# Kernel optimization log

Hardware: AMD Instinct MI355X
Metric: run time of the kernel (lower is better)

Reference implementation:

```python
import jax, jax.numpy as jnp
import numpy as np

B, N, E, F, H, K, C, G = 64, 2048, 16384, 32, 64, 8, 16, 64


def setup_inputs() -> dict:
    key = jax.random.key(0)
    ks = jax.random.split(key, 10)
    s = lambda fan: 1.0 / np.sqrt(fan)
    return {
        "x": jax.random.normal(ks[0], (B, N, C), jnp.float32),
        "linc": (jax.random.uniform(ks[1], (N, E)) < (8.0 / N)).astype(jnp.float32),
        "rinc": (jax.random.uniform(ks[2], (E, N)) < (8.0 / N)).astype(jnp.float32),
        "ef": jax.random.normal(ks[3], (E, F), jnp.float32),
        "w1": jax.random.uniform(ks[4], (H, F), jnp.float32, -s(F), s(F)),
        "b1": jax.random.uniform(ks[5], (H,), jnp.float32, -s(F), s(F)),
        "w2": jax.random.uniform(ks[6], (K, H), jnp.float32, -s(H), s(H)),
        "b2": jax.random.uniform(ks[7], (K,), jnp.float32, -s(H), s(H)),
        "gcw": jax.random.uniform(ks[8], (G, C * K), jnp.float32, -s(C * K), s(C * K)),
        "gcb": jax.random.uniform(ks[9], (G,), jnp.float32, -s(C * K), s(C * K)),
    }


def reference(x, linc, rinc, ef, w1, b1, w2, b2, gcw, gcb):
    # edge MLP -> per-edge kernel weights [E, K]
    h = jax.nn.relu(ef @ w1.T + b1)
    w = h @ w2.T + b2
    # structurally: y_k = linc @ diag(w[:,k]) @ rinc @ x, without building [K,N,N]
    z = jnp.einsum('en,bnc->bec', rinc, x)                  # gather: node -> edge
    y = jnp.einsum('ne,ek,bec->bnck', linc, w, z)           # scale + scatter: edge -> node
    b = x.shape[0]
    y = y.reshape(b, N, C * K)                              # matches permute(0,2,-1,1).reshape
    out = jax.nn.relu(y @ gcw.T + gcb)                      # [B, N, G]
    return out.reshape(b, -1)
```

## Files before the change

kernel.cpp:

```cpp
#include <hip/hip_runtime.h>
#include <hip/hip_bf16.h>

#define B_ 64
#define N_ 2048
#define E_ 16384
#define F_ 32
#define H_ 64
#define K_ 8
#define C_ 16
#define G_ 64
#define CK 128
#define CAP 120
#define RCAP 32
#define YLD 136
#define BC 1024

typedef __attribute__((ext_vector_type(8))) short bf16x8;
typedef __attribute__((ext_vector_type(8))) unsigned short u16x8;
typedef __attribute__((ext_vector_type(4))) float f32x4;

__device__ inline float bf2f(unsigned short u) {
  union { unsigned int i; float f; } v; v.i = ((unsigned int)u) << 16; return v.f;
}
__device__ inline unsigned short f2bf(float f) {
  union { float f; unsigned int i; } v; v.f = f;
  unsigned int x = v.i;
  return (unsigned short)((x + 0x7fffu + ((x >> 16) & 1u)) >> 16);
}

__global__ __launch_bounds__(256) void prep_k(
    const float* __restrict__ x, const float* __restrict__ gcw,
    const float* __restrict__ ef, const float* __restrict__ w1,
    const float* __restrict__ b1, const float* __restrict__ w2,
    const float* __restrict__ b2, const float* __restrict__ linc,
    unsigned short* __restrict__ x_t, unsigned short* __restrict__ gcw_bf,
    float* __restrict__ w_out, int* __restrict__ lcnt,
    unsigned short* __restrict__ lidx) {
  int t = threadIdx.x;
  int blk = blockIdx.x;

  if (blk < N_) {
    int n = blk;
    int b = t >> 2, c0 = (t & 3) * 4;
    f32x4 xv = __builtin_nontemporal_load(
        (const f32x4*)(x + (size_t)b*(N_*C_) + (size_t)n*C_ + c0));
    ushort4 o;
    o.x = f2bf(xv.x); o.y = f2bf(xv.y); o.z = f2bf(xv.z); o.w = f2bf(xv.w);
    *(ushort4*)&x_t[(size_t)n*BC + 4*t] = o;
    return;
  }
  if (blk == N_) {
    for (int i = t; i < G_*CK; i += 256) gcw_bf[i] = f2bf(gcw[i]);
    return;
  }
  if (blk <= N_ + E_/256) {
    __shared__ float s_w1[H_*F_];
    __shared__ float s_w2[K_*H_];
    __shared__ float s_b1[H_];
    __shared__ float s_b2[K_];
    for (int i = t; i < H_*F_; i += 256) s_w1[i] = w1[i];
    for (int i = t; i < K_*H_; i += 256) s_w2[i] = w2[i];
    if (t < H_) s_b1[t] = b1[t];
    if (t < K_) s_b2[t] = b2[t];
    __syncthreads();
    int e = (blk - N_ - 1)*256 + t;
    float efr[F_];
    const float4* efp = (const float4*)(ef + (size_t)e*F_);
    #pragma unroll
    for (int f4 = 0; f4 < F_/4; f4++) {
      float4 v = efp[f4];
      efr[f4*4+0]=v.x; efr[f4*4+1]=v.y; efr[f4*4+2]=v.z; efr[f4*4+3]=v.w;
    }
    float acc[K_];
    #pragma unroll
    for (int k = 0; k < K_; k++) acc[k] = s_b2[k];
    #pragma unroll 4
    for (int h = 0; h < H_; h++) {
      float hv = s_b1[h];
      #pragma unroll
      for (int f = 0; f < F_; f++) hv = fmaf(efr[f], s_w1[h*F_+f], hv);
      hv = fmaxf(hv, 0.f);
      #pragma unroll
      for (int k = 0; k < K_; k++) acc[k] = fmaf(hv, s_w2[k*H_+h], acc[k]);
    }
    #pragma unroll
    for (int k = 0; k < K_; k++) w_out[(size_t)e*K_ + k] = acc[k];
    return;
  }
  {
    __shared__ unsigned short s_list[CAP];
    __shared__ int s_cnt;
    int n = blk - (N_ + E_/256 + 1);
    if (t == 0) s_cnt = 0;
    __syncthreads();
    const f32x4* row = (const f32x4*)(linc + (size_t)n*E_);
    #pragma unroll
    for (int j = 0; j < E_/4/256; j++) {
      int i = t + 256*j;
      f32x4 v = __builtin_nontemporal_load(row + i);
      if (v.x != 0.f) { int p = atomicAdd(&s_cnt,1); if (p<CAP) s_list[p] = (unsigned short)(i*4+0); }
      if (v.y != 0.f) { int p = atomicAdd(&s_cnt,1); if (p<CAP) s_list[p] = (unsigned short)(i*4+1); }
      if (v.z != 0.f) { int p = atomicAdd(&s_cnt,1); if (p<CAP) s_list[p] = (unsigned short)(i*4+2); }
      if (v.w != 0.f) { int p = atomicAdd(&s_cnt,1); if (p<CAP) s_list[p] = (unsigned short)(i*4+3); }
    }
    __syncthreads();
    int cnt = min(s_cnt, CAP);
    if (t == 0) lcnt[n] = cnt;
    for (int i = t; i < cnt; i += 256) lidx[(size_t)n*CAP + i] = s_list[i];
  }
}

__global__ __launch_bounds__(256) void scan_gather_k(
    const float* __restrict__ rinc, const unsigned short* __restrict__ x_t,
    unsigned short* __restrict__ z) {
  __shared__ unsigned short s_list[8][RCAP];
  __shared__ int s_cnt[8];
  int t = threadIdx.x;
  int e0 = blockIdx.x * 8;
  if (t < 8) s_cnt[t] = 0;
  __syncthreads();
  const f32x4* base = (const f32x4*)(rinc + (size_t)e0*N_);
  #pragma unroll
  for (int j = 0; j < 8*N_/4/256; j++) {
    int i = t + 256*j;
    f32x4 v = __builtin_nontemporal_load(base + i);
    int er = i >> 9;
    int nn = (i & 511) * 4;
    if (v.x != 0.f) { int p = atomicAdd(&s_cnt[er],1); if (p<RCAP) s_list[er][p] = (unsigned short)(nn+0); }
    if (v.y != 0.f) { int p = atomicAdd(&s_cnt[er],1); if (p<RCAP) s_list[er][p] = (unsigned short)(nn+1); }
    if (v.z != 0.f) { int p = atomicAdd(&s_cnt[er],1); if (p<RCAP) s_list[er][p] = (unsigned short)(nn+2); }
    if (v.w != 0.f) { int p = atomicAdd(&s_cnt[er],1); if (p<RCAP) s_list[er][p] = (unsigned short)(nn+3); }
  }
  __syncthreads();
  int wv = t >> 6, lane = t & 63;
  const unsigned short* xb = x_t + 16*lane;
  #pragma unroll
  for (int rep = 0; rep < 2; rep++) {
    int er = wv + 4*rep;
    int e = e0 + er;
    int cnt = min(s_cnt[er], RCAP);
    float acc[16];
    #pragma unroll
    for (int k = 0; k < 16; k++) acc[k] = 0.f;
    #pragma unroll 2
    for (int i = 0; i < cnt; i++) {
      int n = s_list[er][i];
      u16x8 a0 = *(const u16x8*)(xb + (size_t)n*BC);
      u16x8 a1 = *(const u16x8*)(xb + (size_t)n*BC + 8);
      #pragma unroll
      for (int k = 0; k < 8; k++) { acc[k] += bf2f(a0[k]); acc[8+k] += bf2f(a1[k]); }
    }
    u16x8 o0, o1;
    #pragma unroll
    for (int k = 0; k < 8; k++) { o0[k] = f2bf(acc[k]); o1[k] = f2bf(acc[8+k]); }
    unsigned short* zp = z + (size_t)e*BC + 16*lane;
    __builtin_nontemporal_store(o0, (u16x8*)zp);
    __builtin_nontemporal_store(o1, (u16x8*)(zp + 8));
  }
}

__global__ __launch_bounds__(256, 6) void node_out_k(
    const int* __restrict__ lcnt, const unsigned short* __restrict__ lidx,
    const unsigned short* __restrict__ z, const float* __restrict__ w,
    const unsigned short* __restrict__ gcw_bf, const float* __restrict__ gcb,
    float* __restrict__ out) {
  __shared__ unsigned short s_y[B_*YLD];
  __shared__ float s_w[CAP*K_];
  __shared__ float s_gcb[G_];
  __shared__ int   s_idx[CAP];
  int t = threadIdx.x;
  int n = blockIdx.x;
  if (t < G_) s_gcb[t] = gcb[t];

  int cnt = min(lcnt[n], CAP);
  const unsigned short* lrow = lidx + (size_t)n*CAP;
  for (int i = t; i < cnt; i += 256) s_idx[i] = lrow[i];
  __syncthreads();
  for (int i = t; i < cnt*K_; i += 256)
    s_w[i] = w[(size_t)s_idx[i >> 3]*K_ + (i & 7)];
  __syncthreads();

  float acc[4][K_];
  #pragma unroll
  for (int j = 0; j < 4; j++)
    #pragma unroll
    for (int k = 0; k < K_; k++) acc[j][k] = 0.f;
  const unsigned short* zt = z + 4*t;
  int i = 0;
  for (; i + 4 <= cnt; i += 4) {
    int e0 = s_idx[i], e1 = s_idx[i+1], e2 = s_idx[i+2], e3 = s_idx[i+3];
    ushort4 zu0 = *(const ushort4*)(zt + (size_t)e0*BC);
    ushort4 zu1 = *(const ushort4*)(zt + (size_t)e1*BC);
    ushort4 zu2 = *(const ushort4*)(zt + (size_t)e2*BC);
    ushort4 zu3 = *(const ushort4*)(zt + (size_t)e3*BC);
    #pragma unroll
    for (int u = 0; u < 4; u++) {
      ushort4 zu = (u==0) ? zu0 : (u==1) ? zu1 : (u==2) ? zu2 : zu3;
      const float4* wp = (const float4*)&s_w[(i+u)*K_];
      float4 w0 = wp[0], w1v = wp[1];
      float we[K_] = {w0.x, w0.y, w0.z, w0.w, w1v.x, w1v.y, w1v.z, w1v.w};
      float zv[4] = {bf2f(zu.x), bf2f(zu.y), bf2f(zu.z), bf2f(zu.w)};
      #pragma unroll
      for (int j = 0; j < 4; j++)
        #pragma unroll
        for (int k = 0; k < K_; k++) acc[j][k] = fmaf(zv[j], we[k], acc[j][k]);
    }
  }
  for (; i < cnt; i++) {
    int e = s_idx[i];
    const float4* wp = (const float4*)&s_w[i*K_];
    float4 w0 = wp[0], w1v = wp[1];
    float we[K_] = {w0.x, w0.y, w0.z, w0.w, w1v.x, w1v.y, w1v.z, w1v.w};
    ushort4 zu = *(const ushort4*)(zt + (size_t)e*BC);
    float zv[4] = {bf2f(zu.x), bf2f(zu.y), bf2f(zu.z), bf2f(zu.w)};
    #pragma unroll
    for (int j = 0; j < 4; j++)
      #pragma unroll
      for (int k = 0; k < K_; k++) acc[j][k] = fmaf(zv[j], we[k], acc[j][k]);
  }
  {
    int b = t >> 2, ckb = (t & 3) * 32;
    #pragma unroll
    for (int j = 0; j < 4; j++) {
      ushort4 lo, hi;
      lo.x = f2bf(acc[j][0]); lo.y = f2bf(acc[j][1]); lo.z = f2bf(acc[j][2]); lo.w = f2bf(acc[j][3]);
      hi.x = f2bf(acc[j][4]); hi.y = f2bf(acc[j][5]); hi.z = f2bf(acc[j][6]); hi.w = f2bf(acc[j][7]);
      *(ushort4*)&s_y[b*YLD + ckb + 8*j]     = lo;
      *(ushort4*)&s_y[b*YLD + ckb + 8*j + 4] = hi;
    }
  }
  __syncthreads();

  {
    int wv = t >> 6, lane = t & 63;
    int m = lane & 15, q = lane >> 4;
    f32x4 cf0 = {0.f,0.f,0.f,0.f}, cf1 = cf0, cf2 = cf0, cf3 = cf0;
    #pragma unroll
    for (int ks = 0; ks < 4; ks++) {
      bf16x8 a = *(const bf16x8*)&s_y[(16*wv + m)*YLD + 32*ks + 8*q];
      bf16x8 b0 = *(const bf16x8*)&gcw_bf[(size_t)(m     )*CK + 32*ks + 8*q];
      bf16x8 b1 = *(const bf16x8*)&gcw_bf[(size_t)(16 + m)*CK + 32*ks + 8*q];
      bf16x8 b2 = *(const bf16x8*)&gcw_bf[(size_t)(32 + m)*CK + 32*ks + 8*q];
      bf16x8 b3 = *(const bf16x8*)&gcw_bf[(size_t)(48 + m)*CK + 32*ks + 8*q];
      cf0 = __builtin_amdgcn_mfma_f32_16x16x32_bf16(a, b0, cf0, 0, 0, 0);
      cf1 = __builtin_amdgcn_mfma_f32_16x16x32_bf16(a, b1, cf1, 0, 0, 0);
      cf2 = __builtin_amdgcn_mfma_f32_16x16x32_bf16(a, b2, cf2, 0, 0, 0);
      cf3 = __builtin_amdgcn_mfma_f32_16x16x32_bf16(a, b3, cf3, 0, 0, 0);
    }
    float* ob = out + (size_t)n*G_;
    #pragma unroll
    for (int r = 0; r < 4; r++) {
      int b = 16*wv + 4*q + r;
      float* op = ob + (size_t)b*(N_*G_);
      float v0 = fmaxf(cf0[r] + s_gcb[m],      0.f);
      float v1 = fmaxf(cf1[r] + s_gcb[16 + m], 0.f);
      float v2 = fmaxf(cf2[r] + s_gcb[32 + m], 0.f);
      float v3 = fmaxf(cf3[r] + s_gcb[48 + m], 0.f);
      op[m]      = v0;
      op[16 + m] = v1;
      op[32 + m] = v2;
      op[48 + m] = v3;
    }
  }
}

extern "C" void kernel_launch(void* const* d_in, const int* in_sizes, int n_in,
                              void* d_out, int out_size, void* d_ws, size_t ws_size,
                              hipStream_t stream) {
  const float* x    = (const float*)d_in[0];
  const float* linc = (const float*)d_in[1];
  const float* rinc = (const float*)d_in[2];
  const float* ef   = (const float*)d_in[3];
  const float* w1   = (const float*)d_in[4];
  const float* b1   = (const float*)d_in[5];
  const float* w2   = (const float*)d_in[6];
  const float* b2   = (const float*)d_in[7];
  const float* gcw  = (const float*)d_in[8];
  const float* gcb  = (const float*)d_in[9];
  float* out = (float*)d_out;

  char* ws = (char*)d_ws;
  float* w_e             = (float*)ws;            ws += (size_t)E_*K_*sizeof(float);
  unsigned short* z      = (unsigned short*)ws;   ws += (size_t)E_*BC*sizeof(short);
  unsigned short* x_t    = (unsigned short*)ws;   ws += (size_t)N_*BC*sizeof(short);
  unsigned short* gcw_bf = (unsigned short*)ws;   ws += (size_t)G_*CK*sizeof(short);
  int* lcnt              = (int*)ws;              ws += (size_t)N_*sizeof(int);
  unsigned short* lidx   = (unsigned short*)ws;   ws += (size_t)N_*CAP*sizeof(short);

  prep_k<<<N_ + 1 + E_/256 + N_, 256, 0, stream>>>(
      x, gcw, ef, w1, b1, w2, b2, linc, x_t, gcw_bf, w_e, lcnt, lidx);
  scan_gather_k<<<E_/8, 256, 0, stream>>>(rinc, x_t, z);
  node_out_k<<<N_, 256, 0, stream>>>(lcnt, lidx, z, w_e, gcw_bf, gcb, out);
}
```

Before: 360.2 us.

## Rebalance kernels: run linc scan and edge MLP alongside the rinc gather

Moves the linc row scan and the edge MLP out of the prep kernel into the gather kernel's grid, so the prep kernel only transposes x and converts gcw. The two large dense streams, rinc (for the gather) and linc, now run concurrently in one launch instead of being split across a dependency boundary, which should improve bandwidth overlap and shorten the critical path. The z stores also change from nontemporal to regular stores, so z may stay in cache for node_out_k. The cost is a more heterogeneous grid, where the long scan blocks can leave a tail.

```diff
diff --git a/kernel.cpp b/kernel.cpp
--- a/kernel.cpp
+++ b/kernel.cpp
@@ -28,32 +28,103 @@
   return (unsigned short)((x + 0x7fffu + ((x >> 16) & 1u)) >> 16);
 }
 
-__global__ __launch_bounds__(256) void prep_k(
+__global__ __launch_bounds__(256) void xpose_k(
     const float* __restrict__ x, const float* __restrict__ gcw,
-    const float* __restrict__ ef, const float* __restrict__ w1,
-    const float* __restrict__ b1, const float* __restrict__ w2,
-    const float* __restrict__ b2, const float* __restrict__ linc,
-    unsigned short* __restrict__ x_t, unsigned short* __restrict__ gcw_bf,
-    float* __restrict__ w_out, int* __restrict__ lcnt,
-    unsigned short* __restrict__ lidx) {
+    unsigned short* __restrict__ x_t, unsigned short* __restrict__ gcw_bf) {
   int t = threadIdx.x;
   int blk = blockIdx.x;
-
-  if (blk < N_) {
-    int n = blk;
-    int b = t >> 2, c0 = (t & 3) * 4;
-    f32x4 xv = __builtin_nontemporal_load(
-        (const f32x4*)(x + (size_t)b*(N_*C_) + (size_t)n*C_ + c0));
-    ushort4 o;
-    o.x = f2bf(xv.x); o.y = f2bf(xv.y); o.z = f2bf(xv.z); o.w = f2bf(xv.w);
-    *(ushort4*)&x_t[(size_t)n*BC + 4*t] = o;
-    return;
-  }
   if (blk == N_) {
     for (int i = t; i < G_*CK; i += 256) gcw_bf[i] = f2bf(gcw[i]);
     return;
   }
-  if (blk <= N_ + E_/256) {
+  int n = blk;
+  int b = t >> 2, c0 = (t & 3) * 4;
+  f32x4 xv = __builtin_nontemporal_load(
+      (const f32x4*)(x + (size_t)b*(N_*C_) + (size_t)n*C_ + c0));
+  ushort4 o;
+  o.x = f2bf(xv.x); o.y = f2bf(xv.y); o.z = f2bf(xv.z); o.w = f2bf(xv.w);
+  *(ushort4*)&x_t[(size_t)n*BC + 4*t] = o;
+}
+
+__global__ __launch_bounds__(256) void streams_k(
+    const float* __restrict__ rinc, const unsigned short* __restrict__ x_t,
+    unsigned short* __restrict__ z, const float* __restrict__ linc,
+    int* __restrict__ lcnt, unsigned short* __restrict__ lidx,
+    const float* __restrict__ ef, const float* __restrict__ w1,
+    const float* __restrict__ b1, const float* __restrict__ w2,
+    const float* __restrict__ b2, float* __restrict__ w_out) {
+  int t = threadIdx.x;
+  int blk = blockIdx.x;
+
+  if (blk < E_/8) {
+    __shared__ unsigned short s_list[8][RCAP];
+    __shared__ int s_cnt[8];
+    int e0 = blk * 8;
+    if (t < 8) s_cnt[t] = 0;
+    __syncthreads();
+    const f32x4* base = (const f32x4*)(rinc + (size_t)e0*N_);
+    #pragma unroll
+    for (int j = 0; j < 8*N_/4/256; j++) {
+      int i = t + 256*j;
+      f32x4 v = __builtin_nontemporal_load(base + i);
+      int er = i >> 9;
+      int nn = (i & 511) * 4;
+      if (v.x != 0.f) { int p = atomicAdd(&s_cnt[er],1); if (p<RCAP) s_list[er][p] = (unsigned short)(nn+0); }
+      if (v.y != 0.f) { int p = atomicAdd(&s_cnt[er],1); if (p<RCAP) s_list[er][p] = (unsigned short)(nn+1); }
+      if (v.z != 0.f) { int p = atomicAdd(&s_cnt[er],1); if (p<RCAP) s_list[er][p] = (unsigned short)(nn+2); }
+      if (v.w != 0.f) { int p = atomicAdd(&s_cnt[er],1); if (p<RCAP) s_list[er][p] = (unsigned short)(nn+3); }
+    }
+    __syncthreads();
+    int wv = t >> 6, lane = t & 63;
+    const unsigned short* xb = x_t + 16*lane;
+    #pragma unroll
+    for (int rep = 0; rep < 2; rep++) {
+      int er = wv + 4*rep;
+      int e = e0 + er;
+      int cnt = min(s_cnt[er], RCAP);
+      float acc[16];
+      #pragma unroll
+      for (int k = 0; k < 16; k++) acc[k] = 0.f;
+      #pragma unroll 2
+      for (int i = 0; i < cnt; i++) {
+        int n = s_list[er][i];
+        u16x8 a0 = *(const u16x8*)(xb + (size_t)n*BC);
+        u16x8 a1 = *(const u16x8*)(xb + (size_t)n*BC + 8);
+        #pragma unroll
+        for (int k = 0; k < 8; k++) { acc[k] += bf2f(a0[k]); acc[8+k] += bf2f(a1[k]); }
+      }
+      u16x8 o0, o1;
+      #pragma unroll
+      for (int k = 0; k < 8; k++) { o0[k] = f2bf(acc[k]); o1[k] = f2bf(acc[8+k]); }
+      unsigned short* zp = z + (size_t)e*BC + 16*lane;
+      *(u16x8*)zp = o0;
+      *(u16x8*)(zp + 8) = o1;
+    }
+    return;
+  }
+  if (blk < E_/8 + N_) {
+    __shared__ unsigned short s_list[CAP];
+    __shared__ int s_cnt;
+    int n = blk - E_/8;
+    if (t == 0) s_cnt = 0;
+    __syncthreads();
+    const f32x4* row = (const f32x4*)(linc + (size_t)n*E_);
+    #pragma unroll
+    for (int j = 0; j < E_/4/256; j++) {
+      int i = t + 256*j;
+      f32x4 v = __builtin_nontemporal_load(row + i);
+      if (v.x != 0.f) { int p = atomicAdd(&s_cnt,1); if (p<CAP) s_list[p] = (unsigned short)(i*4+0); }
+      if (v.y != 0.f) { int p = atomicAdd(&s_cnt,1); if (p<CAP) s_list[p] = (unsigned short)(i*4+1); }
+      if (v.z != 0.f) { int p = atomicAdd(&s_cnt,1); if (p<CAP) s_list[p] = (unsigned short)(i*4+2); }
+      if (v.w != 0.f) { int p = atomicAdd(&s_cnt,1); if (p<CAP) s_list[p] = (unsigned short)(i*4+3); }
+    }
+    __syncthreads();
+    int cnt = min(s_cnt, CAP);
+    if (t == 0) lcnt[n] = cnt;
+    for (int i = t; i < cnt; i += 256) lidx[(size_t)n*CAP + i] = s_list[i];
+    return;
+  }
+  {
     __shared__ float s_w1[H_*F_];
     __shared__ float s_w2[K_*H_];
     __shared__ float s_b1[H_];
@@ -63,7 +134,7 @@
     if (t < H_) s_b1[t] = b1[t];
     if (t < K_) s_b2[t] = b2[t];
     __syncthreads();
-    int e = (blk - N_ - 1)*256 + t;
+    int e = (blk - E_/8 - N_)*256 + t;
     float efr[F_];
     const float4* efp = (const float4*)(ef + (size_t)e*F_);
     #pragma unroll
@@ -85,77 +156,6 @@
     }
     #pragma unroll
     for (int k = 0; k < K_; k++) w_out[(size_t)e*K_ + k] = acc[k];
-    return;
-  }
-  {
-    __shared__ unsigned short s_list[CAP];
-    __shared__ int s_cnt;
-    int n = blk - (N_ + E_/256 + 1);
-    if (t == 0) s_cnt = 0;
-    __syncthreads();
-    const f32x4* row = (const f32x4*)(linc + (size_t)n*E_);
-    #pragma unroll
-    for (int j = 0; j < E_/4/256; j++) {
-      int i = t + 256*j;
-      f32x4 v = __builtin_nontemporal_load(row + i);
-      if (v.x != 0.f) { int p = atomicAdd(&s_cnt,1); if (p<CAP) s_list[p] = (unsigned short)(i*4+0); }
-      if (v.y != 0.f) { int p = atomicAdd(&s_cnt,1); if (p<CAP) s_list[p] = (unsigned short)(i*4+1); }
-      if (v.z != 0.f) { int p = atomicAdd(&s_cnt,1); if (p<CAP) s_list[p] = (unsigned short)(i*4+2); }
-      if (v.w != 0.f) { int p = atomicAdd(&s_cnt,1); if (p<CAP) s_list[p] = (unsigned short)(i*4+3); }
-    }
-    __syncthreads();
-    int cnt = min(s_cnt, CAP);
-    if (t == 0) lcnt[n] = cnt;
-    for (int i = t; i < cnt; i += 256) lidx[(size_t)n*CAP + i] = s_list[i];
-  }
-}
-
-__global__ __launch_bounds__(256) void scan_gather_k(
-    const float* __restrict__ rinc, const unsigned short* __restrict__ x_t,
-    unsigned short* __restrict__ z) {
-  __shared__ unsigned short s_list[8][RCAP];
-  __shared__ int s_cnt[8];
-  int t = threadIdx.x;
-  int e0 = blockIdx.x * 8;
-  if (t < 8) s_cnt[t] = 0;
-  __syncthreads();
-  const f32x4* base = (const f32x4*)(rinc + (size_t)e0*N_);
-  #pragma unroll
-  for (int j = 0; j < 8*N_/4/256; j++) {
-    int i = t + 256*j;
-    f32x4 v = __builtin_nontemporal_load(base + i);
-    int er = i >> 9;
-    int nn = (i & 511) * 4;
-    if (v.x != 0.f) { int p = atomicAdd(&s_cnt[er],1); if (p<RCAP) s_list[er][p] = (unsigned short)(nn+0); }
-    if (v.y != 0.f) { int p = atomicAdd(&s_cnt[er],1); if (p<RCAP) s_list[er][p] = (unsigned short)(nn+1); }
-    if (v.z != 0.f) { int p = atomicAdd(&s_cnt[er],1); if (p<RCAP) s_list[er][p] = (unsigned short)(nn+2); }
-    if (v.w != 0.f) { int p = atomicAdd(&s_cnt[er],1); if (p<RCAP) s_list[er][p] = (unsigned short)(nn+3); }
-  }
-  __syncthreads();
-  int wv = t >> 6, lane = t & 63;
-  const unsigned short* xb = x_t + 16*lane;
-  #pragma unroll
-  for (int rep = 0; rep < 2; rep++) {
-    int er = wv + 4*rep;
-    int e = e0 + er;
-    int cnt = min(s_cnt[er], RCAP);
-    float acc[16];
-    #pragma unroll
-    for (int k = 0; k < 16; k++) acc[k] = 0.f;
-    #pragma unroll 2
-    for (int i = 0; i < cnt; i++) {
-      int n = s_list[er][i];
-      u16x8 a0 = *(const u16x8*)(xb + (size_t)n*BC);
-      u16x8 a1 = *(const u16x8*)(xb + (size_t)n*BC + 8);
-      #pragma unroll
-      for (int k = 0; k < 8; k++) { acc[k] += bf2f(a0[k]); acc[8+k] += bf2f(a1[k]); }
-    }
-    u16x8 o0, o1;
-    #pragma unroll
-    for (int k = 0; k < 8; k++) { o0[k] = f2bf(acc[k]); o1[k] = f2bf(acc[8+k]); }
-    unsigned short* zp = z + (size_t)e*BC + 16*lane;
-    __builtin_nontemporal_store(o0, (u16x8*)zp);
-    __builtin_nontemporal_store(o1, (u16x8*)(zp + 8));
   }
 }
 
@@ -287,8 +287,8 @@
   int* lcnt              = (int*)ws;              ws += (size_t)N_*sizeof(int);
   unsigned short* lidx   = (unsigned short*)ws;   ws += (size_t)N_*CAP*sizeof(short);
 
-  prep_k<<<N_ + 1 + E_/256 + N_, 256, 0, stream>>>(
-      x, gcw, ef, w1, b1, w2, b2, linc, x_t, gcw_bf, w_e, lcnt, lidx);
-  scan_gather_k<<<E_/8, 256, 0, stream>>>(rinc, x_t, z);
+  xpose_k<<<N_ + 1, 256, 0, stream>>>(x, gcw, x_t, gcw_bf);
+  streams_k<<<E_/8 + N_ + E_/256, 256, 0, stream>>>(
+      rinc, x_t, z, linc, lcnt, lidx, ef, w1, b1, w2, b2, w_e);
   node_out_k<<<N_, 256, 0, stream>>>(lcnt, lidx, z, w_e, gcw_bf, gcb, out);
 }
```

Result: slower. 379.7 us (+5.4%).
